# Kernel tuning notes

Measured on AMD Instinct MI355X. Metric: run time of the kernel, lower is better.

Reference implementation:

```python
import jax, jax.numpy as jnp
import numpy as np

N = 100000   # nodes
E = 3200000  # edges (avg degree 32)
NFEAT, NHID, NCLASS = 256, 128, 16


def setup_inputs() -> dict:
    key = jax.random.key(0)
    ks = jax.random.split(key, 8)
    x = jax.random.normal(ks[0], (N, NFEAT), dtype=jnp.float32)
    W1 = jax.random.normal(ks[1], (NFEAT, NHID), dtype=jnp.float32) / np.sqrt(NFEAT)
    b1 = jnp.zeros((NHID,), dtype=jnp.float32)
    W2 = jax.random.normal(ks[2], (NHID, NCLASS), dtype=jnp.float32) / np.sqrt(NHID)
    b2 = jnp.zeros((NCLASS,), dtype=jnp.float32)
    edge_weight = jax.random.uniform(ks[3], (E,), dtype=jnp.float32)
    src = jax.random.randint(ks[4], (E,), 0, N, dtype=jnp.int32)
    dst = jax.random.randint(ks[5], (E,), 0, N, dtype=jnp.int32)
    return {"x": x, "W1": W1, "b1": b1, "W2": W2, "b2": b2,
            "edge_weight": edge_weight, "src": src, "dst": dst}


def _spmm(edge_weight, src, dst, h):
    # adj @ h with adj given as COO edge list: out[dst] += w * h[src]
    msgs = edge_weight[:, None] * h[src]            # [E, d]
    return jax.ops.segment_sum(msgs, dst, num_segments=N)


def reference(x, W1, b1, W2, b2, edge_weight, src, dst):
    # gc1: spmm(adj, x @ W1) + b1, then relu (dropout is identity in eval)
    h = _spmm(edge_weight, src, dst, x @ W1) + b1   # [N, NHID]
    h = jax.nn.relu(h)
    # gc2: spmm(adj, h @ W2) + b2
    logits = _spmm(edge_weight, src, dst, h @ W2) + b2  # [N, NCLASS]
    return jax.nn.log_softmax(logits, axis=1)
```

## Files before the change

### kernel.cpp

```cpp
#include <hip/hip_runtime.h>

#define NN 100000
#define EE 3200000
#define NF 256
#define NH 128
#define NC 16
#define NBKT 391
#define BSZ 256
#define BCAP 9600
#define CHUNK 4096

typedef __bf16 bf16;
typedef bf16 bf16x2 __attribute__((ext_vector_type(2)));
typedef bf16 bf16x4 __attribute__((ext_vector_type(4)));
typedef bf16 bf16x8 __attribute__((ext_vector_type(8)));
typedef float f32x2 __attribute__((ext_vector_type(2)));
typedef float f32x4 __attribute__((ext_vector_type(4)));


__global__ void k_init(int* __restrict__ bucket_cursor, int2* __restrict__ edges) {
    int t = threadIdx.x;
    if (t < NBKT) bucket_cursor[t] = t * BCAP;
    if (t >= 480) edges[EE + t - 480] = make_int2(0, 0);
}

__global__ __launch_bounds__(512) void k_bucket(const int* __restrict__ src,
                                                const int* __restrict__ dst,
                                                const float* __restrict__ ew,
                                                int* __restrict__ bucket_cursor,
                                                int2* __restrict__ staged) {
    __shared__ int2 recs[CHUNK];
    __shared__ int sdst[CHUNK];
    __shared__ unsigned short bkt[CHUNK];
    __shared__ int cnt[NBKT], start[NBKT + 1], cur[NBKT], gbase[NBKT];
    __shared__ int sc[512];
    int t = threadIdx.x;
    int base = blockIdx.x * CHUNK;
    int n = EE - base; if (n > CHUNK) n = CHUNK;
    if (t < NBKT) cnt[t] = 0;
    __syncthreads();
    for (int i = t; i < n; i += 512) {
        int d = dst[base + i];
        sdst[i] = d;
        atomicAdd(&cnt[d >> 8], 1);
    }
    __syncthreads();
    sc[t] = (t < NBKT) ? cnt[t] : 0;
    __syncthreads();
    for (int off = 1; off < 512; off <<= 1) {
        int v = (t >= off) ? sc[t - off] : 0;
        __syncthreads();
        sc[t] += v;
        __syncthreads();
    }
    if (t < NBKT) { start[t] = sc[t] - cnt[t]; cur[t] = sc[t] - cnt[t]; }
    if (t == 0) start[NBKT] = sc[511];
    __syncthreads();
    for (int i = t; i < n; i += 512) {
        int d = sdst[i];
        int b = d >> 8;
        int p = atomicAdd(&cur[b], 1);
        recs[p] = make_int2(src[base + i] | ((d & 255) << 17), __float_as_int(ew[base + i]));
        bkt[p] = (unsigned short)b;
    }
    __syncthreads();
    if (t < NBKT) gbase[t] = atomicAdd(&bucket_cursor[t], start[t + 1] - start[t]);
    __syncthreads();
    for (int i = t; i < n; i += 512) {
        int b = bkt[i];
        staged[gbase[b] + (i - start[b])] = recs[i];
    }
}

__global__ void k_bscan(const int* __restrict__ bucket_cursor,
                        int* __restrict__ bucket_base, int* __restrict__ row_off) {
    __shared__ int s[512];
    int t = threadIdx.x;
    int v = (t < NBKT) ? (bucket_cursor[t] - t * BCAP) : 0;
    s[t] = v;
    __syncthreads();
    for (int off = 1; off < 512; off <<= 1) {
        int x = (t >= off) ? s[t - off] : 0;
        __syncthreads();
        s[t] += x;
        __syncthreads();
    }
    if (t < NBKT) bucket_base[t] = s[t] - v;
    if (t == 0) { bucket_base[NBKT] = EE; row_off[NN] = EE; }
}

__global__ void k_cvtW1(const float* __restrict__ W1, bf16* __restrict__ W1T) {
    int i = blockIdx.x * 256 + threadIdx.x;
    int k = i >> 7, n = i & 127;
    W1T[n * NF + k] = (bf16)W1[i];
}


union SortGemmSmem {
    struct {
        int2 lrec[BCAP];
        int lcnt[BSZ], lstart[BSZ], lcur[BSZ];
    } s;
    unsigned short sW[NH * NF];
};

__device__ __forceinline__ void sort_body(SortGemmSmem& u, int b,
                                          const int2* __restrict__ staged,
                                          const int* __restrict__ bucket_cursor,
                                          const int* __restrict__ bucket_base,
                                          int* __restrict__ row_off,
                                          int2* __restrict__ edges) {
    int t = threadIdx.x;
    int n = bucket_cursor[b] - b * BCAP;
    int gb = bucket_base[b];
    const int2* sp = staged + (size_t)b * BCAP;
    if (t < BSZ) u.s.lcnt[t] = 0;
    __syncthreads();
    for (int i = t; i < n; i += 512) {
        int2 r = sp[i];
        u.s.lrec[i] = r;
        atomicAdd(&u.s.lcnt[r.x >> 17], 1);
    }
    __syncthreads();
    if (t < BSZ) u.s.lstart[t] = u.s.lcnt[t];
    __syncthreads();
    for (int off = 1; off < BSZ; off <<= 1) {
        int v = 0;
        if (t < BSZ && t >= off) v = u.s.lstart[t - off];
        __syncthreads();
        if (t < BSZ) u.s.lstart[t] += v;
        __syncthreads();
    }
    if (t < BSZ) {
        int ex = u.s.lstart[t] - u.s.lcnt[t];
        u.s.lcur[t] = ex;
        int node = (b << 8) + t;
        if (node < NN) row_off[node] = gb + ex;
    }
    __syncthreads();
    for (int i = t; i < n; i += 512) {
        int2 r = u.s.lrec[i];
        int d = r.x >> 17;
        int p = atomicAdd(&u.s.lcur[d], 1);
        edges[gb + p] = make_int2(r.x & 0x1FFFF, r.y);
    }
}

__device__ __forceinline__ void gemm1_body(SortGemmSmem& u, int gid,
                                           const float* __restrict__ x,
                                           const bf16* __restrict__ W1T,
                                           unsigned char* __restrict__ h0q) {
    int t = threadIdx.x;
    int lane = t & 63;
    int wid = t >> 6;
    int m = lane & 15;
    int kg = lane >> 4;
    int row = gid * 128 + wid * 16 + m;
    bool in = (row < NN);
    const float* xr = x + (size_t)row * NF;

#pragma unroll
    for (int it = 0; it < 8; it++) {
        int cid = t + it * 512;
        int n = cid >> 5, ch = cid & 31;
        const bf16* srcp = W1T + (size_t)n * NF + ((ch ^ (n & 7)) << 3);
        __builtin_amdgcn_global_load_lds(
            (const __attribute__((address_space(1))) void*)srcp,
            (__attribute__((address_space(3))) void*)&u.sW[cid << 3],
            16, 0, 0);
    }

    bf16x8 a[8];
#pragma unroll
    for (int kt = 0; kt < 8; kt++) {
        int k0 = kt * 32 + kg * 8;
        float4 uu = in ? *(const float4*)(xr + k0)     : make_float4(0.f, 0.f, 0.f, 0.f);
        float4 vv = in ? *(const float4*)(xr + k0 + 4) : make_float4(0.f, 0.f, 0.f, 0.f);
        bf16x8 av = { (bf16)uu.x, (bf16)uu.y, (bf16)uu.z, (bf16)uu.w,
                      (bf16)vv.x, (bf16)vv.y, (bf16)vv.z, (bf16)vv.w };
        a[kt] = av;
    }
    __syncthreads();

    f32x4 acc[8] = {};
#pragma unroll
    for (int ct = 0; ct < 8; ct++) {
        int brow = ct * 16 + m;
        const unsigned short* bp = u.sW + brow * NF;
        int sw = brow & 7;
#pragma unroll
        for (int kt = 0; kt < 8; kt++) {
            int ch = kt * 4 + kg;
            bf16x8 b = *(const bf16x8*)(bp + ((ch ^ sw) << 3));
            acc[ct] = __builtin_amdgcn_mfma_f32_16x16x32_bf16(b, a[kt], acc[ct], 0, 0, 0);
        }
    }

    if (in) {
        unsigned char* rp = h0q + (size_t)row * NH + kg * 4;
#pragma unroll
        for (int ct = 0; ct < 8; ct++) {
            unsigned lo = (unsigned)__builtin_amdgcn_cvt_pk_fp8_f32(
                              acc[ct][0], acc[ct][1], 0, false);
            unsigned pk = (unsigned)__builtin_amdgcn_cvt_pk_fp8_f32(
                              acc[ct][2], acc[ct][3], lo, true);
            *(unsigned*)(rp + ct * 16) = pk;
        }
    }
}

__global__ __launch_bounds__(512, 4) void k_sortgemm1(const int2* __restrict__ staged,
                                                      const int* __restrict__ bucket_cursor,
                                                      const int* __restrict__ bucket_base,
                                                      int* __restrict__ row_off,
                                                      int2* __restrict__ edges,
                                                      const float* __restrict__ x,
                                                      const bf16* __restrict__ W1T,
                                                      unsigned char* __restrict__ h0q) {
    __shared__ SortGemmSmem u;
    int bid = blockIdx.x;
    int r3 = bid % 3;
    if (r3 == 0) sort_body(u, bid / 3, staged, bucket_cursor, bucket_base, row_off, edges);
    else         gemm1_body(u, (bid / 3) * 2 + r3 - 1, x, W1T, h0q);
}


__global__ __launch_bounds__(256) void k_spmm1g(const int* __restrict__ row_off,
                                                const int2* __restrict__ edges,
                                                const unsigned char* __restrict__ h0q,
                                                const float* __restrict__ b1,
                                                const float* __restrict__ W2,
                                                bf16* __restrict__ g) {
    __shared__ float hs[4][NH];
    int wid = __builtin_amdgcn_readfirstlane(threadIdx.x >> 6);
    int node = blockIdx.x * 4 + wid;
    int lane = threadIdx.x & 63;
    int lq = lane & 31;
    bool hhi = lane >= 32;
    int kg = lane >> 4, c = lane & 15;

    float w2r[32];
#pragma unroll
    for (int j = 0; j < 32; j++) w2r[j] = W2[(kg * 32 + j) * NC + c];

    int s = row_off[node], e = row_off[node + 1];
    unsigned loff = (unsigned)lq * 4u;

    float a0[2] = {0.f, 0.f}, a1[2] = {0.f, 0.f};
    float a2[2] = {0.f, 0.f}, a3[2] = {0.f, 0.f};

    for (int i = s; i < e; i += 16) {
        int2 q[16];
#pragma unroll
        for (int j = 0; j < 16; j++) q[j] = edges[i + j];
        unsigned so[8]; float wo[8];
#pragma unroll
        for (int j = 0; j < 8; j++) {
            bool v0 = (i + 2 * j)     < e;
            bool v1 = (i + 2 * j + 1) < e;
            unsigned s0 = v0 ? (unsigned)q[2 * j].x : 0u;
            unsigned s1 = v1 ? (unsigned)q[2 * j + 1].x : 0u;
            float w0 = v0 ? __int_as_float(q[2 * j].y) : 0.f;
            float w1 = v1 ? __int_as_float(q[2 * j + 1].y) : 0.f;
            so[j] = hhi ? s1 : s0;
            wo[j] = hhi ? w1 : w0;
        }
        unsigned dv[8];
#pragma unroll
        for (int j = 0; j < 8; j++) {
            unsigned off = (so[j] << 7) + loff;
            dv[j] = *(const unsigned*)(h0q + off);
        }
#pragma unroll
        for (int j = 0; j < 8; j++) {
            f32x2 f01 = __builtin_amdgcn_cvt_pk_f32_fp8(dv[j], false);
            f32x2 f23 = __builtin_amdgcn_cvt_pk_f32_fp8(dv[j], true);
            int p = j & 1;
            a0[p] += wo[j] * f01[0];
            a1[p] += wo[j] * f01[1];
            a2[p] += wo[j] * f23[0];
            a3[p] += wo[j] * f23[1];
        }
    }
    float t0 = a0[0] + a0[1];
    float t1 = a1[0] + a1[1];
    float t2 = a2[0] + a2[1];
    float t3 = a3[0] + a3[1];
    t0 += __shfl_xor(t0, 32);
    t1 += __shfl_xor(t1, 32);
    t2 += __shfl_xor(t2, 32);
    t3 += __shfl_xor(t3, 32);

    float4 bv = ((const float4*)b1)[lq];
    float r0 = fmaxf(t0 + bv.x, 0.f);
    float r1 = fmaxf(t1 + bv.y, 0.f);
    float r2 = fmaxf(t2 + bv.z, 0.f);
    float r3 = fmaxf(t3 + bv.w, 0.f);
    if (!hhi) *(float4*)&hs[wid][lq * 4] = make_float4(r0, r1, r2, r3);
    const float* hp = &hs[wid][kg * 32];
    float p = 0.f;
#pragma unroll
    for (int j = 0; j < 32; j++) p += hp[j] * w2r[j];
    p += __shfl_xor(p, 16);
    p += __shfl_xor(p, 32);
    if (lane < 16) g[(size_t)node * NC + lane] = (bf16)p;
}


__global__ __launch_bounds__(256) void k_spmm2(const int* __restrict__ row_off,
                                               const int2* __restrict__ edges,
                                               const bf16* __restrict__ g,
                                               const float* __restrict__ b2,
                                               float* __restrict__ out) {
    int node = (blockIdx.x * 256 + threadIdx.x) >> 6;
    int lane = threadIdx.x & 63;
    int grp = lane >> 3, l = lane & 7;
    int s = row_off[node], e = row_off[node + 1];
    const char* gb = (const char*)g;
    unsigned coff = (unsigned)l * 4u;

    float a0 = 0.f, a1 = 0.f;
    for (int i = s; i < e; i += 16) {
        int i0 = i + grp, i1 = i0 + 8;
        int2 r0 = edges[i0];
        int2 r1 = edges[i1];
        bool v0 = i0 < e, v1 = i1 < e;
        unsigned s0 = v0 ? (unsigned)r0.x : 0u;
        float    w0 = v0 ? __int_as_float(r0.y) : 0.f;
        unsigned s1 = v1 ? (unsigned)r1.x : 0u;
        float    w1 = v1 ? __int_as_float(r1.y) : 0.f;
        unsigned d0 = *(const unsigned*)(gb + ((s0 << 5) + coff));
        unsigned d1 = *(const unsigned*)(gb + ((s1 << 5) + coff));
        a0 += w0 * __int_as_float(d0 << 16);
        a1 += w0 * __int_as_float(d0 & 0xffff0000u);
        a0 += w1 * __int_as_float(d1 << 16);
        a1 += w1 * __int_as_float(d1 & 0xffff0000u);
    }
    a0 += __shfl_xor(a0, 8);  a1 += __shfl_xor(a1, 8);
    a0 += __shfl_xor(a0, 16); a1 += __shfl_xor(a1, 16);
    a0 += __shfl_xor(a0, 32); a1 += __shfl_xor(a1, 32);
    float2 bv = ((const float2*)b2)[l];
    a0 += bv.x; a1 += bv.y;
    float m = fmaxf(a0, a1);
    m = fmaxf(m, __shfl_xor(m, 1));
    m = fmaxf(m, __shfl_xor(m, 2));
    m = fmaxf(m, __shfl_xor(m, 4));
    float e0 = __expf(a0 - m), e1 = __expf(a1 - m);
    float sum = e0 + e1;
    sum += __shfl_xor(sum, 1);
    sum += __shfl_xor(sum, 2);
    sum += __shfl_xor(sum, 4);
    float ls = __logf(sum);
    if (l == lane && lane < 8) {
        float2 o = { a0 - m - ls, a1 - m - ls };
        *(float2*)(out + (size_t)node * NC + 2 * l) = o;
    }
}


extern "C" void kernel_launch(void* const* d_in, const int* in_sizes, int n_in,
                              void* d_out, int out_size, void* d_ws, size_t ws_size,
                              hipStream_t stream) {
    const float* x  = (const float*)d_in[0];
    const float* W1 = (const float*)d_in[1];
    const float* b1 = (const float*)d_in[2];
    const float* W2 = (const float*)d_in[3];
    const float* b2 = (const float*)d_in[4];
    const float* ew = (const float*)d_in[5];
    const int* src  = (const int*)d_in[6];
    const int* dst  = (const int*)d_in[7];
    float* out = (float*)d_out;

    char* ws = (char*)d_ws;
    unsigned char* h0q = (unsigned char*)(ws + 0);
    bf16*  g       = (bf16*)(ws + 12800000);
    int*   row_off = (int*)(ws + 16000000);
    int*   bucket_cursor = (int*)(ws + 16400016);
    int*   bucket_base   = (int*)(ws + 16401584);
    int2*  edges   = (int2*)(ws + 16403168);
    bf16*  W1T     = (bf16*)(ws + 42003424);
    int2*  staged  = (int2*)(ws + 42068960);

    k_init<<<1, 512, 0, stream>>>(bucket_cursor, edges);
    k_cvtW1<<<(NF * NH) / 256, 256, 0, stream>>>(W1, W1T);
    k_bucket<<<(EE + CHUNK - 1) / CHUNK, 512, 0, stream>>>(src, dst, ew, bucket_cursor, staged);
    k_bscan<<<1, 512, 0, stream>>>(bucket_cursor, bucket_base, row_off);

    k_sortgemm1<<<1173, 512, 0, stream>>>(staged, bucket_cursor, bucket_base,
                                          row_off, edges, x, W1T, h0q);

    k_spmm1g<<<NN / 4, 256, 0, stream>>>(row_off, edges, h0q, b1, W2, g);

    k_spmm2<<<NN / 4, 256, 0, stream>>>(row_off, edges, g, b2, out);
}
```

Before: 372.1 us.

## Shrink sort/GEMM shared memory to raise occupancy and split GEMM columns

The fused sort+GEMM1 kernel drops its LDS staging buffer of edge records and re-reads them from global memory, and each GEMM block now computes only half of the 128 output columns, so the W1 tile in LDS halves. The smaller LDS footprint and per-tile accumulators allow 6 blocks per CU instead of 4, with the grid reshaped to a 1:4 sort/GEMM interleave. It also halves the bucketing chunk size and merges the init and W1 transpose kernels into one launch. In exchange, x rows are loaded twice (once per column half), staged records are read twice from global memory, and bucket-cursor atomics increase with more chunks.

```diff
diff --git a/kernel.cpp b/kernel.cpp
--- a/kernel.cpp
+++ b/kernel.cpp
@@ -8,7 +8,7 @@
 #define NBKT 391
 #define BSZ 256
 #define BCAP 9600
-#define CHUNK 4096
+#define CHUNK 2048
 
 typedef __bf16 bf16;
 typedef bf16 bf16x2 __attribute__((ext_vector_type(2)));
@@ -18,11 +18,19 @@
 typedef float f32x4 __attribute__((ext_vector_type(4)));
 
 
-__global__ void k_init(int* __restrict__ bucket_cursor, int2* __restrict__ edges) {
-    int t = threadIdx.x;
-    if (t < NBKT) bucket_cursor[t] = t * BCAP;
-    if (t >= 480) edges[EE + t - 480] = make_int2(0, 0);
-}
+__global__ void k_prep(const float* __restrict__ W1, bf16* __restrict__ W1T,
+                       int* __restrict__ bucket_cursor, int2* __restrict__ edges) {
+    int b = blockIdx.x, t = threadIdx.x;
+    if (b < 128) {
+        int i = b * 256 + t;
+        int k = i >> 7, n = i & 127;
+        W1T[n * NF + k] = (bf16)W1[i];
+    } else {
+        for (int i = t; i < NBKT; i += 256) bucket_cursor[i] = i * BCAP;
+        if (t < 32) edges[EE + t] = make_int2(0, 0);
+    }
+}
+
 
 __global__ __launch_bounds__(512) void k_bucket(const int* __restrict__ src,
                                                 const int* __restrict__ dst,
@@ -89,19 +97,12 @@
     if (t == 0) { bucket_base[NBKT] = EE; row_off[NN] = EE; }
 }
 
-__global__ void k_cvtW1(const float* __restrict__ W1, bf16* __restrict__ W1T) {
-    int i = blockIdx.x * 256 + threadIdx.x;
-    int k = i >> 7, n = i & 127;
-    W1T[n * NF + k] = (bf16)W1[i];
-}
-
 
 union SortGemmSmem {
     struct {
-        int2 lrec[BCAP];
         int lcnt[BSZ], lstart[BSZ], lcur[BSZ];
     } s;
-    unsigned short sW[NH * NF];
+    unsigned short sW[64 * NF];
 };
 
 __device__ __forceinline__ void sort_body(SortGemmSmem& u, int b,
@@ -117,9 +118,8 @@
     if (t < BSZ) u.s.lcnt[t] = 0;
     __syncthreads();
     for (int i = t; i < n; i += 512) {
-        int2 r = sp[i];
-        u.s.lrec[i] = r;
-        atomicAdd(&u.s.lcnt[r.x >> 17], 1);
+        int sx = sp[i].x;
+        atomicAdd(&u.s.lcnt[sx >> 17], 1);
     }
     __syncthreads();
     if (t < BSZ) u.s.lstart[t] = u.s.lcnt[t];
@@ -139,7 +139,7 @@
     }
     __syncthreads();
     for (int i = t; i < n; i += 512) {
-        int2 r = u.s.lrec[i];
+        int2 r = sp[i];
         int d = r.x >> 17;
         int p = atomicAdd(&u.s.lcur[d], 1);
         edges[gb + p] = make_int2(r.x & 0x1FFFF, r.y);
@@ -155,15 +155,17 @@
     int wid = t >> 6;
     int m = lane & 15;
     int kg = lane >> 4;
-    int row = gid * 128 + wid * 16 + m;
+    int half = gid & 1;
+    int row = (gid >> 1) * 128 + wid * 16 + m;
     bool in = (row < NN);
     const float* xr = x + (size_t)row * NF;
-
-#pragma unroll
-    for (int it = 0; it < 8; it++) {
+    const bf16* wbase = W1T + (size_t)half * 64 * NF;
+
+#pragma unroll
+    for (int it = 0; it < 4; it++) {
         int cid = t + it * 512;
         int n = cid >> 5, ch = cid & 31;
-        const bf16* srcp = W1T + (size_t)n * NF + ((ch ^ (n & 7)) << 3);
+        const bf16* srcp = wbase + (size_t)n * NF + ((ch ^ (n & 7)) << 3);
         __builtin_amdgcn_global_load_lds(
             (const __attribute__((address_space(1))) void*)srcp,
             (__attribute__((address_space(3))) void*)&u.sW[cid << 3],
@@ -182,9 +184,10 @@
     }
     __syncthreads();
 
-    f32x4 acc[8] = {};
-#pragma unroll
-    for (int ct = 0; ct < 8; ct++) {
+    unsigned char* rp = h0q + (size_t)row * NH + half * 64 + kg * 4;
+#pragma unroll
+    for (int ct = 0; ct < 4; ct++) {
+        f32x4 acc = {};
         int brow = ct * 16 + m;
         const unsigned short* bp = u.sW + brow * NF;
         int sw = brow & 7;
@@ -192,24 +195,17 @@
         for (int kt = 0; kt < 8; kt++) {
             int ch = kt * 4 + kg;
             bf16x8 b = *(const bf16x8*)(bp + ((ch ^ sw) << 3));
-            acc[ct] = __builtin_amdgcn_mfma_f32_16x16x32_bf16(b, a[kt], acc[ct], 0, 0, 0);
-        }
-    }
-
-    if (in) {
-        unsigned char* rp = h0q + (size_t)row * NH + kg * 4;
-#pragma unroll
-        for (int ct = 0; ct < 8; ct++) {
-            unsigned lo = (unsigned)__builtin_amdgcn_cvt_pk_fp8_f32(
-                              acc[ct][0], acc[ct][1], 0, false);
-            unsigned pk = (unsigned)__builtin_amdgcn_cvt_pk_fp8_f32(
-                              acc[ct][2], acc[ct][3], lo, true);
+            acc = __builtin_amdgcn_mfma_f32_16x16x32_bf16(b, a[kt], acc, 0, 0, 0);
+        }
+        if (in) {
+            unsigned lo = (unsigned)__builtin_amdgcn_cvt_pk_fp8_f32(acc[0], acc[1], 0, false);
+            unsigned pk = (unsigned)__builtin_amdgcn_cvt_pk_fp8_f32(acc[2], acc[3], lo, true);
             *(unsigned*)(rp + ct * 16) = pk;
         }
     }
 }
 
-__global__ __launch_bounds__(512, 4) void k_sortgemm1(const int2* __restrict__ staged,
+__global__ __launch_bounds__(512, 6) void k_sortgemm1(const int2* __restrict__ staged,
                                                       const int* __restrict__ bucket_cursor,
                                                       const int* __restrict__ bucket_base,
                                                       int* __restrict__ row_off,
@@ -219,9 +215,9 @@
                                                       unsigned char* __restrict__ h0q) {
     __shared__ SortGemmSmem u;
     int bid = blockIdx.x;
-    int r3 = bid % 3;
-    if (r3 == 0) sort_body(u, bid / 3, staged, bucket_cursor, bucket_base, row_off, edges);
-    else         gemm1_body(u, (bid / 3) * 2 + r3 - 1, x, W1T, h0q);
+    int r5 = bid % 5;
+    if (r5 == 0) sort_body(u, bid / 5, staged, bucket_cursor, bucket_base, row_off, edges);
+    else         gemm1_body(u, (bid / 5) * 4 + r5 - 1, x, W1T, h0q);
 }
 
 
@@ -381,12 +377,11 @@
     bf16*  W1T     = (bf16*)(ws + 42003424);
     int2*  staged  = (int2*)(ws + 42068960);
 
-    k_init<<<1, 512, 0, stream>>>(bucket_cursor, edges);
-    k_cvtW1<<<(NF * NH) / 256, 256, 0, stream>>>(W1, W1T);
+    k_prep<<<129, 256, 0, stream>>>(W1, W1T, bucket_cursor, edges);
     k_bucket<<<(EE + CHUNK - 1) / CHUNK, 512, 0, stream>>>(src, dst, ew, bucket_cursor, staged);
     k_bscan<<<1, 512, 0, stream>>>(bucket_cursor, bucket_base, row_off);
 
-    k_sortgemm1<<<1173, 512, 0, stream>>>(staged, bucket_cursor, bucket_base,
+    k_sortgemm1<<<1955, 512, 0, stream>>>(staged, bucket_cursor, bucket_base,
                                           row_off, edges, x, W1T, h0q);
 
     k_spmm1g<<<NN / 4, 256, 0, stream>>>(row_off, edges, h0q, b1, W2, g);
```

Measured after the change: 400.0 us. +7.5%, slower.

## Co-schedule edge bucketing with GEMM1 and merge init with W1 conversion

Applied to the files above, without the earlier changes.

Merges the init and W1-transpose kernels into a single prep kernel. The GEMM1 blocks are now interleaved with the edge-bucketing pass instead of the per-bucket sort pass, and the sort becomes its own kernel after the bucket scan. The aim is to hide the bandwidth-bound bucketing work behind the compute-bound GEMM and to cut launch count. The cost is that the sort now runs alone without GEMM overlap, and the fused kernel's shared-memory union changes size, which may affect occupancy.

```diff
diff --git a/kernel.cpp b/kernel.cpp
--- a/kernel.cpp
+++ b/kernel.cpp
@@ -18,57 +18,16 @@
 typedef float f32x4 __attribute__((ext_vector_type(4)));
 
 
-__global__ void k_init(int* __restrict__ bucket_cursor, int2* __restrict__ edges) {
-    int t = threadIdx.x;
-    if (t < NBKT) bucket_cursor[t] = t * BCAP;
-    if (t >= 480) edges[EE + t - 480] = make_int2(0, 0);
-}
-
-__global__ __launch_bounds__(512) void k_bucket(const int* __restrict__ src,
-                                                const int* __restrict__ dst,
-                                                const float* __restrict__ ew,
-                                                int* __restrict__ bucket_cursor,
-                                                int2* __restrict__ staged) {
-    __shared__ int2 recs[CHUNK];
-    __shared__ int sdst[CHUNK];
-    __shared__ unsigned short bkt[CHUNK];
-    __shared__ int cnt[NBKT], start[NBKT + 1], cur[NBKT], gbase[NBKT];
-    __shared__ int sc[512];
-    int t = threadIdx.x;
-    int base = blockIdx.x * CHUNK;
-    int n = EE - base; if (n > CHUNK) n = CHUNK;
-    if (t < NBKT) cnt[t] = 0;
-    __syncthreads();
-    for (int i = t; i < n; i += 512) {
-        int d = dst[base + i];
-        sdst[i] = d;
-        atomicAdd(&cnt[d >> 8], 1);
-    }
-    __syncthreads();
-    sc[t] = (t < NBKT) ? cnt[t] : 0;
-    __syncthreads();
-    for (int off = 1; off < 512; off <<= 1) {
-        int v = (t >= off) ? sc[t - off] : 0;
-        __syncthreads();
-        sc[t] += v;
-        __syncthreads();
-    }
-    if (t < NBKT) { start[t] = sc[t] - cnt[t]; cur[t] = sc[t] - cnt[t]; }
-    if (t == 0) start[NBKT] = sc[511];
-    __syncthreads();
-    for (int i = t; i < n; i += 512) {
-        int d = sdst[i];
-        int b = d >> 8;
-        int p = atomicAdd(&cur[b], 1);
-        recs[p] = make_int2(src[base + i] | ((d & 255) << 17), __float_as_int(ew[base + i]));
-        bkt[p] = (unsigned short)b;
-    }
-    __syncthreads();
-    if (t < NBKT) gbase[t] = atomicAdd(&bucket_cursor[t], start[t + 1] - start[t]);
-    __syncthreads();
-    for (int i = t; i < n; i += 512) {
-        int b = bkt[i];
-        staged[gbase[b] + (i - start[b])] = recs[i];
+__global__ void k_prep(const float* __restrict__ W1, bf16* __restrict__ W1T,
+                       int* __restrict__ bucket_cursor, int2* __restrict__ edges) {
+    int b = blockIdx.x, t = threadIdx.x;
+    if (b < 128) {
+        int i = b * 256 + t;
+        int k = i >> 7, n = i & 127;
+        W1T[n * NF + k] = (bf16)W1[i];
+    } else {
+        for (int i = t; i < NBKT; i += 256) bucket_cursor[i] = i * BCAP;
+        if (t < 32) edges[EE + t] = make_int2(0, 0);
     }
 }
 
@@ -89,64 +48,63 @@
     if (t == 0) { bucket_base[NBKT] = EE; row_off[NN] = EE; }
 }
 
-__global__ void k_cvtW1(const float* __restrict__ W1, bf16* __restrict__ W1T) {
-    int i = blockIdx.x * 256 + threadIdx.x;
-    int k = i >> 7, n = i & 127;
-    W1T[n * NF + k] = (bf16)W1[i];
-}
-
-
-union SortGemmSmem {
+
+union BucketGemmSmem {
     struct {
-        int2 lrec[BCAP];
-        int lcnt[BSZ], lstart[BSZ], lcur[BSZ];
-    } s;
+        int2 recs[CHUNK];
+        int sdst[CHUNK];
+        unsigned short bkt[CHUNK];
+        int cnt[NBKT], start[NBKT + 1], cur[NBKT], gbase[NBKT];
+        int sc[512];
+    } b;
     unsigned short sW[NH * NF];
 };
 
-__device__ __forceinline__ void sort_body(SortGemmSmem& u, int b,
-                                          const int2* __restrict__ staged,
-                                          const int* __restrict__ bucket_cursor,
-                                          const int* __restrict__ bucket_base,
-                                          int* __restrict__ row_off,
-                                          int2* __restrict__ edges) {
+__device__ __forceinline__ void bucket_body(BucketGemmSmem& u, int cid,
+                                            const int* __restrict__ src,
+                                            const int* __restrict__ dst,
+                                            const float* __restrict__ ew,
+                                            int* __restrict__ bucket_cursor,
+                                            int2* __restrict__ staged) {
     int t = threadIdx.x;
-    int n = bucket_cursor[b] - b * BCAP;
-    int gb = bucket_base[b];
-    const int2* sp = staged + (size_t)b * BCAP;
-    if (t < BSZ) u.s.lcnt[t] = 0;
-    __syncthreads();
-    for (int i = t; i < n; i += 512) {
-        int2 r = sp[i];
-        u.s.lrec[i] = r;
-        atomicAdd(&u.s.lcnt[r.x >> 17], 1);
-    }
-    __syncthreads();
-    if (t < BSZ) u.s.lstart[t] = u.s.lcnt[t];
-    __syncthreads();
-    for (int off = 1; off < BSZ; off <<= 1) {
-        int v = 0;
-        if (t < BSZ && t >= off) v = u.s.lstart[t - off];
-        __syncthreads();
-        if (t < BSZ) u.s.lstart[t] += v;
-        __syncthreads();
-    }
-    if (t < BSZ) {
-        int ex = u.s.lstart[t] - u.s.lcnt[t];
-        u.s.lcur[t] = ex;
-        int node = (b << 8) + t;
-        if (node < NN) row_off[node] = gb + ex;
-    }
-    __syncthreads();
-    for (int i = t; i < n; i += 512) {
-        int2 r = u.s.lrec[i];
-        int d = r.x >> 17;
-        int p = atomicAdd(&u.s.lcur[d], 1);
-        edges[gb + p] = make_int2(r.x & 0x1FFFF, r.y);
-    }
-}
-
-__device__ __forceinline__ void gemm1_body(SortGemmSmem& u, int gid,
+    int base = cid * CHUNK;
+    int n = EE - base; if (n > CHUNK) n = CHUNK;
+    if (t < NBKT) u.b.cnt[t] = 0;
+    __syncthreads();
+    for (int i = t; i < n; i += 512) {
+        int d = dst[base + i];
+        u.b.sdst[i] = d;
+        atomicAdd(&u.b.cnt[d >> 8], 1);
+    }
+    __syncthreads();
+    u.b.sc[t] = (t < NBKT) ? u.b.cnt[t] : 0;
+    __syncthreads();
+    for (int off = 1; off < 512; off <<= 1) {
+        int v = (t >= off) ? u.b.sc[t - off] : 0;
+        __syncthreads();
+        u.b.sc[t] += v;
+        __syncthreads();
+    }
+    if (t < NBKT) { u.b.start[t] = u.b.sc[t] - u.b.cnt[t]; u.b.cur[t] = u.b.sc[t] - u.b.cnt[t]; }
+    if (t == 0) u.b.start[NBKT] = u.b.sc[511];
+    __syncthreads();
+    for (int i = t; i < n; i += 512) {
+        int d = u.b.sdst[i];
+        int b = d >> 8;
+        int p = atomicAdd(&u.b.cur[b], 1);
+        u.b.recs[p] = make_int2(src[base + i] | ((d & 255) << 17), __float_as_int(ew[base + i]));
+        u.b.bkt[p] = (unsigned short)b;
+    }
+    __syncthreads();
+    if (t < NBKT) u.b.gbase[t] = atomicAdd(&bucket_cursor[t], u.b.start[t + 1] - u.b.start[t]);
+    __syncthreads();
+    for (int i = t; i < n; i += 512) {
+        int b = u.b.bkt[i];
+        staged[u.b.gbase[b] + (i - u.b.start[b])] = u.b.recs[i];
+    }
+}
+
+__device__ __forceinline__ void gemm1_body(BucketGemmSmem& u, int gid,
                                            const float* __restrict__ x,
                                            const bf16* __restrict__ W1T,
                                            unsigned char* __restrict__ h0q) {
@@ -209,19 +167,63 @@
     }
 }
 
-__global__ __launch_bounds__(512, 4) void k_sortgemm1(const int2* __restrict__ staged,
-                                                      const int* __restrict__ bucket_cursor,
-                                                      const int* __restrict__ bucket_base,
-                                                      int* __restrict__ row_off,
-                                                      int2* __restrict__ edges,
-                                                      const float* __restrict__ x,
-                                                      const bf16* __restrict__ W1T,
-                                                      unsigned char* __restrict__ h0q) {
-    __shared__ SortGemmSmem u;
+__global__ __launch_bounds__(512, 4) void k_bucketgemm1(const int* __restrict__ src,
+                                                        const int* __restrict__ dst,
+                                                        const float* __restrict__ ew,
+                                                        int* __restrict__ bucket_cursor,
+                                                        int2* __restrict__ staged,
+                                                        const float* __restrict__ x,
+                                                        const bf16* __restrict__ W1T,
+                                                        unsigned char* __restrict__ h0q) {
+    __shared__ BucketGemmSmem u;
     int bid = blockIdx.x;
-    int r3 = bid % 3;
-    if (r3 == 0) sort_body(u, bid / 3, staged, bucket_cursor, bucket_base, row_off, edges);
-    else         gemm1_body(u, (bid / 3) * 2 + r3 - 1, x, W1T, h0q);
+    if (bid & 1) gemm1_body(u, bid >> 1, x, W1T, h0q);
+    else         bucket_body(u, bid >> 1, src, dst, ew, bucket_cursor, staged);
+}
+
+
+__global__ __launch_bounds__(512) void k_sort(const int2* __restrict__ staged,
+                                              const int* __restrict__ bucket_cursor,
+                                              const int* __restrict__ bucket_base,
+                                              int* __restrict__ row_off,
+                                              int2* __restrict__ edges) {
+    __shared__ int2 lrec[BCAP];
+    __shared__ int lcnt[BSZ], lstart[BSZ], lcur[BSZ];
+    int t = threadIdx.x;
+    int b = blockIdx.x;
+    int n = bucket_cursor[b] - b * BCAP;
+    int gb = bucket_base[b];
+    const int2* sp = staged + (size_t)b * BCAP;
+    if (t < BSZ) lcnt[t] = 0;
+    __syncthreads();
+    for (int i = t; i < n; i += 512) {
+        int2 r = sp[i];
+        lrec[i] = r;
+        atomicAdd(&lcnt[r.x >> 17], 1);
+    }
+    __syncthreads();
+    if (t < BSZ) lstart[t] = lcnt[t];
+    __syncthreads();
+    for (int off = 1; off < BSZ; off <<= 1) {
+        int v = 0;
+        if (t < BSZ && t >= off) v = lstart[t - off];
+        __syncthreads();
+        if (t < BSZ) lstart[t] += v;
+        __syncthreads();
+    }
+    if (t < BSZ) {
+        int ex = lstart[t] - lcnt[t];
+        lcur[t] = ex;
+        int node = (b << 8) + t;
+        if (node < NN) row_off[node] = gb + ex;
+    }
+    __syncthreads();
+    for (int i = t; i < n; i += 512) {
+        int2 r = lrec[i];
+        int d = r.x >> 17;
+        int p = atomicAdd(&lcur[d], 1);
+        edges[gb + p] = make_int2(r.x & 0x1FFFF, r.y);
+    }
 }
 
 
@@ -381,13 +383,12 @@
     bf16*  W1T     = (bf16*)(ws + 42003424);
     int2*  staged  = (int2*)(ws + 42068960);
 
-    k_init<<<1, 512, 0, stream>>>(bucket_cursor, edges);
-    k_cvtW1<<<(NF * NH) / 256, 256, 0, stream>>>(W1, W1T);
-    k_bucket<<<(EE + CHUNK - 1) / CHUNK, 512, 0, stream>>>(src, dst, ew, bucket_cursor, staged);
+    k_prep<<<129, 256, 0, stream>>>(W1, W1T, bucket_cursor, edges);
+
+    k_bucketgemm1<<<1564, 512, 0, stream>>>(src, dst, ew, bucket_cursor, staged,
+                                            x, W1T, h0q);
     k_bscan<<<1, 512, 0, stream>>>(bucket_cursor, bucket_base, row_off);
-
-    k_sortgemm1<<<1173, 512, 0, stream>>>(staged, bucket_cursor, bucket_base,
-                                          row_off, edges, x, W1T, h0q);
+    k_sort<<<NBKT, 512, 0, stream>>>(staged, bucket_cursor, bucket_base, row_off, edges);
 
     k_spmm1g<<<NN / 4, 256, 0, stream>>>(row_off, edges, h0q, b1, W2, g);
 
```

New measurement: 363.6 us. 2.3% less time.
